# Performance work log

Hardware: AMD Instinct MI355X
Metric: run time of the kernel (lower is better)

## Reference

```python
import jax, jax.numpy as jnp
import numpy as np
import math

B, S, SIG, EMB, LAT, H, L_ENC, L_DEC = 16, 1024, 256, 256, 256, 8, 2, 2
EH, DH = EMB // H, LAT // H
EPS = 1e-10


def _sinusoidal_last_row(d):
    # last row of a standard sinusoidal PE table (position index = max_len-1)
    pos = 5000.0 - 1.0
    i = np.arange(d)
    angles = pos / np.power(10000.0, (2 * (i // 2)) / d)
    pe = np.where(i % 2 == 0, np.sin(angles), np.cos(angles))
    return jnp.asarray(pe, dtype=jnp.float32)


def setup_inputs() -> dict:
    key = jax.random.key(0)
    ks = iter(jax.random.split(key, 64))
    w = lambda *sh: 0.05 * jax.random.normal(next(ks), sh, dtype=jnp.float32)
    z = lambda *sh: jnp.zeros(sh, dtype=jnp.float32)
    d = {
        'inputData': jax.random.normal(next(ks), (B, S, SIG), dtype=jnp.float32),
        'pos_enc': _sinusoidal_last_row(SIG),
        'embW': w(SIG, EMB), 'embb': z(EMB),
        'qW': w(EMB, EMB), 'qb': z(EMB),
        'kW': w(EMB, EMB), 'kb': z(EMB),
        'vW': w(EMB, EMB), 'vb': z(EMB),
        'encBW': w(EH, EH), 'encBb': z(EH),
        'oW': w(EMB, EMB), 'ob': z(EMB),
        'ffe_W1': w(EMB, 2 * EMB), 'ffe_b1': z(2 * EMB),
        'ffe_W2': w(2 * EMB, EMB), 'ffe_b2': z(EMB),
        'lnSA_g': jnp.ones((L_ENC, EMB)), 'lnSA_b': z(L_ENC, EMB),
        'lnFF_g': jnp.ones((L_ENC, EMB)), 'lnFF_b': z(L_ENC, EMB),
        'start': w(1, LAT),
        'decQW': w(LAT, LAT), 'decQb': z(LAT),
        'decKW': w(EMB, EMB), 'decKb': z(EMB),
        'decVW': w(EMB, LAT), 'decVb': z(LAT),
        'decBW': w(EH + DH, DH), 'decBb': z(DH),
        'latW': w(LAT, LAT), 'latb': z(LAT),
        'ffd_W1': w(LAT, LAT // 2), 'ffd_b1': z(LAT // 2),
        'ffd_W2': w(LAT // 2, LAT), 'ffd_b2': z(LAT),
        'lnCA_g': jnp.ones((L_DEC, LAT)), 'lnCA_b': z(L_DEC, LAT),
        'lnLFF_g': jnp.ones((L_DEC, LAT)), 'lnLFF_b': z(L_DEC, LAT),
        'finW': w(LAT, LAT), 'finb': z(LAT),
    }
    return d


def _ln(x, g, b):
    m = x.mean(-1, keepdims=True)
    v = x.var(-1, keepdims=True)
    return (x - m) * jax.lax.rsqrt(v + EPS) * g + b


def _enc_attn(x, qW, qb, kW, kb, vW, vb, bW, bb, oW, ob):
    # x: (B,S,EMB) -> heads (B,H,S,EH)
    sp = lambda t: t.reshape(B, S, H, EH).transpose(0, 2, 1, 3)
    q, k, v = sp(x @ qW + qb), sp(x @ kW + kb), sp(x @ vW + vb)
    bk = k @ bW + bb                                   # bilinear key (B,H,S,EH)
    attn = jax.nn.softmax(jnp.einsum('bhqd,bhkd->bhqk', q, bk) / math.sqrt(EH), axis=-1)
    out = jnp.einsum('bhqk,bhkd->bhqd', attn, v)
    out = out.transpose(0, 2, 1, 3).reshape(B, S, EMB)
    return out @ oW + ob


def _dec_attn(enc, lat, qW, qb, kW, kb, vW, vb, bW, bb, oW, ob):
    # lat: (B,LAT) single query token; enc: (B,S,EMB)
    q = (lat @ qW + qb).reshape(B, 1, H, DH).transpose(0, 2, 1, 3)   # (B,H,1,DH)
    k = (enc @ kW + kb).reshape(B, S, H, EH).transpose(0, 2, 1, 3)   # (B,H,S,EH)
    v = (enc @ vW + vb).reshape(B, S, H, DH).transpose(0, 2, 1, 3)   # (B,H,S,DH)
    qcat = jnp.broadcast_to(q, (B, H, S, DH))
    kcat = jnp.concatenate([k, qcat], axis=-1)                       # (B,H,S,EH+DH)
    bk = kcat @ bW + bb                                              # (B,H,S,DH)
    attn = jax.nn.softmax(jnp.einsum('bhqd,bhkd->bhqk', q, bk) / math.sqrt(EH + DH), axis=-1)
    out = jnp.einsum('bhqk,bhkd->bhqd', attn, v)                     # (B,H,1,DH)
    out = out.transpose(0, 2, 1, 3).reshape(B, LAT)
    return out @ oW + ob


def reference(inputData, pos_enc, embW, embb, qW, qb, kW, kb, vW, vb, encBW, encBb,
              oW, ob, ffe_W1, ffe_b1, ffe_W2, ffe_b2, lnSA_g, lnSA_b, lnFF_g, lnFF_b,
              start, decQW, decQb, decKW, decKb, decVW, decVb, decBW, decBb,
              latW, latb, ffd_W1, ffd_b1, ffd_W2, ffd_b2, lnCA_g, lnCA_b,
              lnLFF_g, lnLFF_b, finW, finb):
    emb = (inputData + pos_enc) @ embW + embb          # (B,S,EMB)
    t = emb
    for l in range(L_ENC):
        n = _ln(t, lnSA_g[l], lnSA_b[l])
        a = _enc_attn(n, qW, qb, kW, kb, vW, vb, encBW, encBb, oW, ob) + n
        t = a + emb
        n2 = _ln(t, lnFF_g[l], lnFF_b[l])
        ff = jax.nn.selu(n2 @ ffe_W1 + ffe_b1) @ ffe_W2 + ffe_b2
        t = ff + n2
    init_lat = jnp.broadcast_to(start, (B, LAT))
    lat = init_lat
    for l in range(L_DEC):
        nl = _ln(init_lat, lnCA_g[l], lnCA_b[l])       # module always feeds initialLatentData
        lat = _dec_attn(t, nl, decQW, decQb, decKW, decKb, decVW, decVb,
                        decBW, decBb, latW, latb)
        nf = _ln(lat, lnLFF_g[l], lnLFF_b[l])
        lat = jax.nn.selu(nf @ ffd_W1 + ffd_b1) @ ffd_W2 + ffd_b2
    return lat @ finW + finb
```

## Files before the change

kernel.cpp:

```cpp
#include <hip/hip_runtime.h>
#include <hip/hip_bf16.h>
#include <math.h>

typedef __hip_bfloat16 bf16;

#define BB 16
#define SS 1024
#define NH 8
#define NR (BB*SS)
#define SZE ((size_t)NR*256)
#define RS 264
#define HS 520
#define KS2 136

typedef __attribute__((ext_vector_type(8))) short short8;
typedef __attribute__((ext_vector_type(4))) float f32x4;
typedef __attribute__((ext_vector_type(8))) unsigned short u16x8;
typedef __attribute__((ext_vector_type(4))) unsigned short u16x4;

__device__ __forceinline__ float bf2f(bf16 x){ return __bfloat162float(x); }
__device__ __forceinline__ bf16  f2bf(float x){ return __float2bfloat16(x); }
__device__ __forceinline__ unsigned short f2bfu(float x){
  bf16 t = __float2bfloat16(x); return *reinterpret_cast<unsigned short*>(&t);
}
__device__ __forceinline__ float bfu2f(unsigned short u){
  return __uint_as_float(((unsigned)u)<<16);
}

__device__ __forceinline__ float ldT(const float* p, size_t i){ return p[i]; }
__device__ __forceinline__ float ldT(const bf16*  p, size_t i){ return bf2f(p[i]); }
__device__ __forceinline__ void  stT(float* p, size_t i, float v){ p[i] = v; }
__device__ __forceinline__ void  stT(bf16*  p, size_t i, float v){ p[i] = f2bf(v); }

__device__ __forceinline__ float selu_f(float x){
  const float a = 1.6732632423543772f, sc = 1.0507009873554805f;
  return sc * (x > 0.f ? x : a * expm1f(x));
}

struct PtrPack { const void* p[43]; };
struct TabPack { int off[43]; int cnt[43]; int total; };
struct TrTab   { int srcOff[12]; int K[12]; int N[12]; int dstOff[12]; int total; };

__global__ __launch_bounds__(256) void k_canon(PtrPack ptrs, TabPack tab,
    float* __restrict__ dst, int* __restrict__ flagw)
{
  unsigned w0 = ((const unsigned*)ptrs.p[18])[0];
  int isbf = (w0 == 0x3F803F80u) ? 1 : 0;
  if (blockIdx.x == 0 && threadIdx.x == 0) *flagw = isbf;
  __shared__ int so[43], sn[43];
  int tid = threadIdx.x;
  if (tid < 43){ so[tid] = tab.off[tid]; sn[tid] = tab.cnt[tid]; }
  __syncthreads();
  int g = blockIdx.x*256 + tid;
  if (g >= tab.total) return;
  int seg = 1;
  while (seg < 42 && g >= so[seg] + sn[seg]) seg++;
  int li = g - so[seg];
  float v = isbf ? bf2f(((const bf16*)ptrs.p[seg])[li])
                 : ((const float*)ptrs.p[seg])[li];
  dst[g] = v;
}

__global__ __launch_bounds__(256) void k_transW(const float* __restrict__ wt,
    TrTab tt, unsigned short* __restrict__ dst)
{
  int g = blockIdx.x*256 + threadIdx.x;
  if (g >= tt.total) return;
  int seg = 0;
  while (seg < 11 && g >= tt.dstOff[seg] + tt.K[seg]*tt.N[seg]) seg++;
  int li = g - tt.dstOff[seg];
  int K = tt.K[seg], N = tt.N[seg];
  int n = li / K, k = li - n*K;
  dst[g] = f2bfu(wt[tt.srcOff[seg] + (size_t)k*N + n]);
}

template<int K, int LDA, int CT>
__device__ __forceinline__ void wave_gemmN(const unsigned short (*As)[LDA],
    const unsigned short* __restrict__ Wt, int n0, f32x4 acc[4][CT], int lane)
{
  int col = lane & 15, quad = lane >> 4;
  #pragma unroll
  for (int k0 = 0; k0 < K; k0 += 32){
    short8 a[4], b[CT];
    #pragma unroll
    for (int rt = 0; rt < 4; rt++)
      a[rt] = *(const short8*)(&As[rt*16 + col][k0 + quad*8]);
    #pragma unroll
    for (int ct = 0; ct < CT; ct++)
      b[ct] = *(const short8*)(&Wt[(size_t)(n0 + ct*16 + col)*K + k0 + quad*8]);
    #pragma unroll
    for (int rt = 0; rt < 4; rt++)
      #pragma unroll
      for (int ct = 0; ct < CT; ct++)
        acc[rt][ct] = __builtin_amdgcn_mfma_f32_16x16x32_bf16(a[rt], b[ct], acc[rt][ct], 0, 0, 0);
  }
}

template<int K, int LDA, int CT>
__device__ __forceinline__ void wave_gemmM32(const unsigned short (*As)[LDA],
    const unsigned short* __restrict__ Wt, int n0, f32x4 acc[2][CT], int lane)
{
  int col = lane & 15, quad = lane >> 4;
  #pragma unroll
  for (int k0 = 0; k0 < K; k0 += 32){
    short8 a[2], b[CT];
    #pragma unroll
    for (int rt = 0; rt < 2; rt++)
      a[rt] = *(const short8*)(&As[rt*16 + col][k0 + quad*8]);
    #pragma unroll
    for (int ct = 0; ct < CT; ct++)
      b[ct] = *(const short8*)(&Wt[(size_t)(n0 + ct*16 + col)*K + k0 + quad*8]);
    #pragma unroll
    for (int rt = 0; rt < 2; rt++)
      #pragma unroll
      for (int ct = 0; ct < CT; ct++)
        acc[rt][ct] = __builtin_amdgcn_mfma_f32_16x16x32_bf16(a[rt], b[ct], acc[rt][ct], 0, 0, 0);
  }
}

#define ZERO_ACC4(acc)  { _Pragma("unroll") for (int rt=0;rt<4;rt++){ _Pragma("unroll") for (int ct=0;ct<4;ct++) acc[rt][ct] = (f32x4){0.f,0.f,0.f,0.f}; } }
#define ZERO_ACC2(acc)  { _Pragma("unroll") for (int rt=0;rt<4;rt++){ _Pragma("unroll") for (int ct=0;ct<2;ct++) acc[rt][ct] = (f32x4){0.f,0.f,0.f,0.f}; } }
#define ZERO_ACC24(acc) { _Pragma("unroll") for (int rt=0;rt<2;rt++){ _Pragma("unroll") for (int ct=0;ct<4;ct++) acc[rt][ct] = (f32x4){0.f,0.f,0.f,0.f}; } }

#define EPI_BEGIN(e) { int rt = (e)>>4, ct = ((e)>>2)&3, r = (e)&3; \
    int lrow = rt*16 + quad*4 + r; int gcol0 = ct*16 + col; \
    float av = acc[rt][ct][r]; (void)lrow; (void)gcol0; (void)av;
#define EPI_END }

#define EPI32_BEGIN(e) { int rt = (e)>>4, ct = ((e)>>2)&3, r = (e)&3; \
    int lrow = rt*16 + quad*4 + r; int gcol0 = ct*16 + col; \
    float av = acc[rt][ct][r]; (void)lrow; (void)gcol0; (void)av;
#define EPI32_END }

template<int PRE, typename OT>
__global__ __launch_bounds__(256) void k_gemm_mfma(const void* __restrict__ A,
    const int* __restrict__ flagp, const float* __restrict__ pe,
    const unsigned short* __restrict__ Wt, const float* __restrict__ bias,
    OT* __restrict__ out)
{
  __shared__ __align__(16) unsigned short As[64][RS];
  int tid = threadIdx.x;
  int m = blockIdx.x & 255, nh = blockIdx.x >> 8;
  int row0 = m*64;
  if (PRE == 0){
    int f = *flagp;
    for (int jj = 0; jj < 64; jj++){
      int idx = tid + jj*256, row = idx>>8, c = idx&255;
      size_t g = (size_t)(row0+row)*256 + c;
      float x = f ? bf2f(((const bf16*)A)[g]) : ((const float*)A)[g];
      As[row][c] = f2bfu(x + pe[c]);
    }
  } else {
    for (int jj = 0; jj < 64; jj++){
      int idx = tid + jj*256, row = idx>>8, c = idx&255;
      As[row][c] = f2bfu(((const float*)A)[(size_t)(row0+row)*256 + c]);
    }
  }
  __syncthreads();
  int w = tid>>6, lane = tid&63, col = lane&15, quad = lane>>4;
  int n0 = nh*128 + w*32;
  f32x4 acc[4][2];
  ZERO_ACC2(acc);
  wave_gemmN<256, RS, 2>(As, Wt, n0, acc, lane);
  #pragma unroll
  for (int rt = 0; rt < 4; rt++){
    #pragma unroll
    for (int ct = 0; ct < 2; ct++){
      #pragma unroll
      for (int r = 0; r < 4; r++){
        int grow = row0 + rt*16 + quad*4 + r;
        int gcol = n0 + ct*16 + col;
        stT(out, (size_t)grow*256 + gcol, acc[rt][ct][r] + bias[gcol]);
      }
    }
  }
}

__global__ __launch_bounds__(256) void k_decKV(const float* __restrict__ A,
    const unsigned short* __restrict__ KWt, const float* __restrict__ kb,
    const unsigned short* __restrict__ VWt, const float* __restrict__ vb,
    bf16* __restrict__ ko, bf16* __restrict__ vo)
{
  __shared__ __align__(16) unsigned short As[64][RS];
  int tid = threadIdx.x;
  int m = blockIdx.x & 255, nh = blockIdx.x >> 8;
  int row0 = m*64;
  for (int jj = 0; jj < 64; jj++){
    int idx = tid + jj*256, row = idx>>8, c = idx&255;
    As[row][c] = f2bfu(A[(size_t)(row0+row)*256 + c]);
  }
  __syncthreads();
  int w = tid>>6, lane = tid&63, col = lane&15, quad = lane>>4;
  int n0 = nh*128 + w*32;
  f32x4 acc[4][2];
  ZERO_ACC2(acc);
  wave_gemmN<256, RS, 2>(As, KWt, n0, acc, lane);
  #pragma unroll
  for (int rt = 0; rt < 4; rt++){
    #pragma unroll
    for (int ct = 0; ct < 2; ct++){
      #pragma unroll
      for (int r = 0; r < 4; r++){
        int grow = row0 + rt*16 + quad*4 + r;
        int gcol = n0 + ct*16 + col;
        ko[(size_t)grow*256 + gcol] = f2bf(acc[rt][ct][r] + kb[gcol]);
      }
    }
  }
  ZERO_ACC2(acc);
  wave_gemmN<256, RS, 2>(As, VWt, n0, acc, lane);
  #pragma unroll
  for (int rt = 0; rt < 4; rt++){
    #pragma unroll
    for (int ct = 0; ct < 2; ct++){
      #pragma unroll
      for (int r = 0; r < 4; r++){
        int grow = row0 + rt*16 + quad*4 + r;
        int gcol = n0 + ct*16 + col;
        vo[(size_t)grow*256 + gcol] = f2bf(acc[rt][ct][r] + vb[gcol]);
      }
    }
  }
}

__global__ __launch_bounds__(256) void k_qkvbk_mfma(const float* __restrict__ tsrc,
    const float* __restrict__ lng, const float* __restrict__ lnb,
    const unsigned short* __restrict__ qWt, const float* __restrict__ qb,
    const unsigned short* __restrict__ kWt, const float* __restrict__ kb,
    const unsigned short* __restrict__ vWt, const float* __restrict__ vb,
    const unsigned short* __restrict__ encBWt, const float* __restrict__ Bb,
    bf16* __restrict__ qo, bf16* __restrict__ vo, bf16* __restrict__ bko)
{
  __shared__ __align__(16) unsigned short Ns[64][RS];
  __shared__ __align__(16) unsigned short Ks[64][KS2];
  __shared__ float mArr[64], rArr[64];
  int tid = threadIdx.x;
  int m = blockIdx.x & 255, nh = blockIdx.x >> 8;
  int row0 = m*64;
  int b = row0 >> 10, s0 = row0 & 1023;
  {
    int row = tid>>2, l4 = tid&3;
    const float* rp = tsrc + (size_t)(row0+row)*256;
    float s = 0.f, s2 = 0.f;
    for (int c = l4; c < 256; c += 4){ float x = rp[c]; s += x; s2 += x*x; }
    s  += __shfl_down(s, 2, 4);  s  += __shfl_down(s, 1, 4);
    s2 += __shfl_down(s2, 2, 4); s2 += __shfl_down(s2, 1, 4);
    if (l4 == 0){
      float mn = s*(1.f/256.f);
      float v = s2*(1.f/256.f) - mn*mn;
      mArr[row] = mn; rArr[row] = rsqrtf(fmaxf(v,0.f) + 1e-10f);
    }
  }
  __syncthreads();
  for (int jj = 0; jj < 64; jj++){
    int idx = tid + jj*256, row = idx>>8, c = idx&255;
    float x = tsrc[(size_t)(row0+row)*256 + c];
    Ns[row][c] = f2bfu((x - mArr[row])*rArr[row]*lng[c] + lnb[c]);
  }
  __syncthreads();
  int w = tid>>6, lane = tid&63, col = lane&15, quad = lane>>4;
  int n0 = nh*128 + w*32;
  f32x4 acc[4][2];
  ZERO_ACC2(acc);
  wave_gemmN<256, RS, 2>(Ns, qWt, n0, acc, lane);
  #pragma unroll
  for (int rt = 0; rt < 4; rt++){
    #pragma unroll
    for (int ct = 0; ct < 2; ct++){
      #pragma unroll
      for (int r = 0; r < 4; r++){
        int grow = row0 + rt*16 + quad*4 + r;
        int gcol = n0 + ct*16 + col;
        qo[(size_t)grow*256 + gcol] = f2bf(acc[rt][ct][r] + qb[gcol]);
      }
    }
  }
  ZERO_ACC2(acc);
  wave_gemmN<256, RS, 2>(Ns, vWt, n0, acc, lane);
  #pragma unroll
  for (int rt = 0; rt < 4; rt++){
    #pragma unroll
    for (int ct = 0; ct < 2; ct++){
      #pragma unroll
      for (int r = 0; r < 4; r++){
        int grow = row0 + rt*16 + quad*4 + r;
        int gcol = n0 + ct*16 + col;
        vo[(size_t)grow*256 + gcol] = f2bf(acc[rt][ct][r] + vb[gcol]);
      }
    }
  }
  ZERO_ACC2(acc);
  wave_gemmN<256, RS, 2>(Ns, kWt, n0, acc, lane);
  #pragma unroll
  for (int rt = 0; rt < 4; rt++){
    #pragma unroll
    for (int ct = 0; ct < 2; ct++){
      #pragma unroll
      for (int r = 0; r < 4; r++){
        int lrow = rt*16 + quad*4 + r;
        int lcol = w*32 + ct*16 + col;
        Ks[lrow][lcol] = f2bfu(acc[rt][ct][r] + kb[nh*128 + lcol]);
      }
    }
  }
  __syncthreads();
  int h = nh*4 + w;
  ZERO_ACC2(acc);
  #pragma unroll
  for (int ct = 0; ct < 2; ct++){
    short8 bfrag = *(const short8*)(&encBWt[(size_t)(ct*16 + col)*32 + quad*8]);
    #pragma unroll
    for (int rt = 0; rt < 4; rt++){
      short8 afrag = *(const short8*)(&Ks[rt*16 + col][w*32 + quad*8]);
      acc[rt][ct] = __builtin_amdgcn_mfma_f32_16x16x32_bf16(afrag, bfrag, acc[rt][ct], 0, 0, 0);
    }
  }
  #pragma unroll
  for (int rt = 0; rt < 4; rt++){
    #pragma unroll
    for (int ct = 0; ct < 2; ct++){
      #pragma unroll
      for (int r = 0; r < 4; r++){
        int srow = s0 + rt*16 + quad*4 + r;
        int d = ct*16 + col;
        bko[(((size_t)(b*NH+h))*SS + srow)*32 + d] = f2bf(acc[rt][ct][r] + Bb[d]);
      }
    }
  }
}

__global__ __launch_bounds__(256) void k_attn_mfma(
    const bf16* __restrict__ q, const bf16* __restrict__ bk,
    const bf16* __restrict__ v, bf16* __restrict__ ao)
{
  int bi = blockIdx.x;
  int qq = bi >> 7, b = (bi >> 3) & 15, h = bi & 7;
  int tid = threadIdx.x;
  int w = tid>>6, lane = tid&63;
  int quad = lane>>4, col = lane&15;
  int q0 = qq*256 + w*64;

  __shared__ __align__(16) unsigned short Ks2b[2][64][32];
  __shared__ __align__(16) unsigned short Vt2b[2][32][72];
  __shared__ __align__(16) unsigned short Ps[4][64][72];

  const float scale2 = 0.17677669529663687f * 1.4426950408889634f;
  short8 aq[4];
  #pragma unroll
  for (int rt = 0; rt < 4; rt++){
    const unsigned short* gq = (const unsigned short*)q
        + ((size_t)(b*SS + q0 + rt*16 + col))*256 + h*32 + quad*8;
    u16x8 qv = *(const u16x8*)gq;
    #pragma unroll
    for (int i=0;i<8;i++) aq[rt][i] = (short)f2bfu(bfu2f(qv[i])*scale2);
  }

  float l_r[4][4];
  f32x4 o0[4], o1[4];
  #pragma unroll
  for (int rt=0;rt<4;rt++){
    o0[rt] = (f32x4){0.f,0.f,0.f,0.f};
    o1[rt] = (f32x4){0.f,0.f,0.f,0.f};
    #pragma unroll
    for (int r=0;r<4;r++) l_r[rt][r] = 0.f;
  }

  u16x8 rK;
  u16x4 rV0, rV1;
  int vk0 = (tid>>3), vdg = (tid&7);
  int vk1 = ((tid+256)>>3), vdg1 = (tid&7);
  {
    const u16x8* srcK = (const u16x8*)((const unsigned short*)bk
        + (((size_t)(b*NH+h))*SS + 0)*32);
    rK = srcK[tid];
    rV0 = *(const u16x4*)((const unsigned short*)v
        + ((size_t)(b*SS + 0 + vk0))*256 + h*32 + vdg*4);
    rV1 = *(const u16x4*)((const unsigned short*)v
        + ((size_t)(b*SS + 0 + vk1))*256 + h*32 + vdg1*4);
  }

  for (int kt = 0; kt < 16; kt++){
    int cb = kt & 1;
    ((u16x8*)&Ks2b[cb][0][0])[tid] = rK;
    #pragma unroll
    for (int i=0;i<4;i++) Vt2b[cb][vdg*4+i][vk0] = rV0[i];
    #pragma unroll
    for (int i=0;i<4;i++) Vt2b[cb][vdg1*4+i][vk1] = rV1[i];
    __syncthreads();
    if (kt < 15){
      int nk = kt + 1;
      const u16x8* srcK = (const u16x8*)((const unsigned short*)bk
          + (((size_t)(b*NH+h))*SS + (size_t)nk*64)*32);
      rK = srcK[tid];
      rV0 = *(const u16x4*)((const unsigned short*)v
          + ((size_t)(b*SS + nk*64 + vk0))*256 + h*32 + vdg*4);
      rV1 = *(const u16x4*)((const unsigned short*)v
          + ((size_t)(b*SS + nk*64 + vk1))*256 + h*32 + vdg1*4);
    }
    short8 bk8[4];
    #pragma unroll
    for (int t4 = 0; t4 < 4; t4++)
      bk8[t4] = *(const short8*)(&Ks2b[cb][t4*16 + col][quad*8]);
    #pragma unroll
    for (int rt = 0; rt < 4; rt++){
      f32x4 s[4];
      #pragma unroll
      for (int t4 = 0; t4 < 4; t4++)
        s[t4] = __builtin_amdgcn_mfma_f32_16x16x32_bf16(aq[rt], bk8[t4],
                  (f32x4){0.f,0.f,0.f,0.f}, 0, 0, 0);
      #pragma unroll
      for (int r=0;r<4;r++){
        #pragma unroll
        for (int t4=0;t4<4;t4++){
          float pv = __builtin_amdgcn_exp2f(s[t4][r]);
          l_r[rt][r] += pv;
          Ps[w][rt*16 + quad*4 + r][t4*16 + col] =
              (unsigned short)(__float_as_uint(pv) >> 16);
        }
      }
    }
    short8 bv00 = *(const short8*)(&Vt2b[cb][col][quad*8]);
    short8 bv10 = *(const short8*)(&Vt2b[cb][col][32 + quad*8]);
    short8 bv01 = *(const short8*)(&Vt2b[cb][16+col][quad*8]);
    short8 bv11 = *(const short8*)(&Vt2b[cb][16+col][32 + quad*8]);
    #pragma unroll
    for (int rt = 0; rt < 4; rt++){
      short8 ap0 = *(const short8*)(&Ps[w][rt*16 + col][quad*8]);
      short8 ap1 = *(const short8*)(&Ps[w][rt*16 + col][32 + quad*8]);
      o0[rt] = __builtin_amdgcn_mfma_f32_16x16x32_bf16(ap0, bv00, o0[rt], 0, 0, 0);
      o0[rt] = __builtin_amdgcn_mfma_f32_16x16x32_bf16(ap1, bv10, o0[rt], 0, 0, 0);
      o1[rt] = __builtin_amdgcn_mfma_f32_16x16x32_bf16(ap0, bv01, o1[rt], 0, 0, 0);
      o1[rt] = __builtin_amdgcn_mfma_f32_16x16x32_bf16(ap1, bv11, o1[rt], 0, 0, 0);
    }
  }
  #pragma unroll
  for (int rt=0;rt<4;rt++){
    #pragma unroll
    for (int r=0;r<4;r++){
      float l = l_r[rt][r];
      #pragma unroll
      for (int msk=1; msk<16; msk<<=1) l += __shfl_xor(l, msk, 64);
      float inv = 1.f / l;
      int qrow = q0 + rt*16 + quad*4 + r;
      size_t o = ((size_t)(b*SS + qrow))*256 + h*32;
      ao[o + col]      = f2bf(o0[rt][r]*inv);
      ao[o + 16 + col] = f2bf(o1[rt][r]*inv);
    }
  }
}

__global__ __launch_bounds__(256) void k_oln_mfma(
    const float* __restrict__ tsrc, const float* __restrict__ emb,
    const bf16* __restrict__ ao,
    const float* __restrict__ lnSAg, const float* __restrict__ lnSAb,
    const unsigned short* __restrict__ oWt, const float* __restrict__ ob,
    const float* __restrict__ lnFFg, const float* __restrict__ lnFFb,
    bf16* __restrict__ n2o)
{
  __shared__ __align__(16) unsigned short Aos[32][RS];
  __shared__ __align__(16) unsigned short Tm[32][RS];
  __shared__ float mArr[32], rArr[32];
  int tid = threadIdx.x, row0 = blockIdx.x*32;
  {
    int row = tid>>3, l8 = tid&7;
    const float* rp = tsrc + (size_t)(row0+row)*256;
    float s = 0.f, s2 = 0.f;
    for (int c = l8; c < 256; c += 8){ float x = rp[c]; s += x; s2 += x*x; }
    s  += __shfl_down(s, 4, 8);  s  += __shfl_down(s, 2, 8);  s  += __shfl_down(s, 1, 8);
    s2 += __shfl_down(s2, 4, 8); s2 += __shfl_down(s2, 2, 8); s2 += __shfl_down(s2, 1, 8);
    if (l8 == 0){
      float m = s*(1.f/256.f);
      float v = s2*(1.f/256.f) - m*m;
      mArr[row] = m; rArr[row] = rsqrtf(fmaxf(v,0.f) + 1e-10f);
    }
  }
  for (int jj = 0; jj < 4; jj++){
    int idx = tid + jj*256;
    int row = idx>>5, c8 = idx&31;
    *(u16x8*)(&Aos[row][c8*8]) =
        *(const u16x8*)((const unsigned short*)ao + (size_t)(row0+row)*256 + c8*8);
  }
  __syncthreads();
  int w = tid>>6, lane = tid&63, col = lane&15, quad = lane>>4;
  f32x4 acc[2][4];
  ZERO_ACC24(acc);
  wave_gemmM32<256, RS, 4>(Aos, oWt, w*64, acc, lane);
  #pragma unroll
  for (int e = 0; e < 32; e++){
    EPI32_BEGIN(e)
    int gcol = w*64 + gcol0;
    size_t g = (size_t)(row0+lrow)*256 + gcol;
    float n1 = (tsrc[g] - mArr[lrow])*rArr[lrow]*lnSAg[gcol] + lnSAb[gcol];
    Tm[lrow][gcol] = f2bfu(av + ob[gcol] + n1 + emb[g]);
    EPI32_END
  }
  __syncthreads();
  {
    int row = tid>>3, l8 = tid&7;
    float s = 0.f, s2 = 0.f;
    for (int c = l8; c < 256; c += 8){ float x = bfu2f(Tm[row][c]); s += x; s2 += x*x; }
    s  += __shfl_down(s, 4, 8);  s  += __shfl_down(s, 2, 8);  s  += __shfl_down(s, 1, 8);
    s2 += __shfl_down(s2, 4, 8); s2 += __shfl_down(s2, 2, 8); s2 += __shfl_down(s2, 1, 8);
    if (l8 == 0){
      float m = s*(1.f/256.f);
      float v = s2*(1.f/256.f) - m*m;
      mArr[row] = m; rArr[row] = rsqrtf(fmaxf(v,0.f) + 1e-10f);
    }
  }
  __syncthreads();
  for (int jj = 0; jj < 32; jj++){
    int idx = tid + jj*256, row = idx>>8, c = idx&255;
    float x = bfu2f(Tm[row][c]);
    n2o[(size_t)(row0+row)*256 + c] =
        f2bf((x - mArr[row])*rArr[row]*lnFFg[c] + lnFFb[c]);
  }
}

__global__ __launch_bounds__(256) void k_ffn_mfma(
    const bf16* __restrict__ n2,
    const unsigned short* __restrict__ W1t, const float* __restrict__ b1,
    const unsigned short* __restrict__ W2t, const float* __restrict__ b2,
    float* __restrict__ tout)
{
  __shared__ __align__(16) unsigned short N2s[32][RS];
  __shared__ __align__(16) unsigned short H1s[32][HS];
  int tid = threadIdx.x, row0 = blockIdx.x*32;
  for (int jj = 0; jj < 4; jj++){
    int idx = tid + jj*256;
    int row = idx>>5, c8 = idx&31;
    *(u16x8*)(&N2s[row][c8*8]) =
        *(const u16x8*)((const unsigned short*)n2 + (size_t)(row0+row)*256 + c8*8);
  }
  __syncthreads();
  int w = tid>>6, lane = tid&63, col = lane&15, quad = lane>>4;
  f32x4 acc[2][4];
  #pragma unroll
  for (int p = 0; p < 2; p++){
    ZERO_ACC24(acc);
    wave_gemmM32<256, RS, 4>(N2s, W1t, p*256 + w*64, acc, lane);
    #pragma unroll
    for (int e = 0; e < 32; e++){
      EPI32_BEGIN(e)
      int gcol = p*256 + w*64 + gcol0;
      H1s[lrow][gcol] = f2bfu(selu_f(av + b1[gcol]));
      EPI32_END
    }
  }
  __syncthreads();
  ZERO_ACC24(acc);
  wave_gemmM32<512, HS, 4>(H1s, W2t, w*64, acc, lane);
  #pragma unroll
  for (int e = 0; e < 32; e++){
    EPI32_BEGIN(e)
    int gcol = w*64 + gcol0;
    tout[(size_t)(row0+lrow)*256 + gcol] = av + b2[gcol] + bfu2f(N2s[lrow][gcol]);
    EPI32_END
  }
}

__global__ __launch_bounds__(256) void k_dec_head(const float* __restrict__ startp,
    const float* __restrict__ lng, const float* __restrict__ lnb,
    const float* __restrict__ decQW, const float* __restrict__ decQb,
    const float* __restrict__ decBW,
    float* __restrict__ s_q, float* __restrict__ s_qc)
{
  __shared__ float s1[256], s2[256], nl[256], qv[256];
  int t = threadIdx.x;
  float v = startp[t];
  s1[t]=v; s2[t]=v*v; __syncthreads();
  for (int s=128;s>0;s>>=1){
    if (t<s){ s1[t]+=s1[t+s]; s2[t]+=s2[t+s]; }
    __syncthreads();
  }
  float m = s1[0]*(1.f/256.f);
  float var = s2[0]*(1.f/256.f) - m*m;
  float r = rsqrtf(fmaxf(var,0.f) + 1e-10f);
  nl[t] = (v-m)*r*lng[t] + lnb[t];
  __syncthreads();
  float acc = decQb[t];
  for (int k=0;k<256;k++) acc += nl[k]*decQW[k*256+t];
  qv[t] = acc; s_q[t] = acc;
  __syncthreads();
  int h = t>>5, d = t&31;
  float a = 0.f;
  #pragma unroll 8
  for (int e=0;e<32;e++) a += qv[h*32+e]*decBW[(32+e)*32 + d];
  s_qc[t] = a;
}

__global__ __launch_bounds__(256) void k_bkdec_mfma(const bf16* __restrict__ kk,
    const float* __restrict__ qc, const unsigned short* __restrict__ decBWt,
    const float* __restrict__ Bb, bf16* __restrict__ bko)
{
  __shared__ __align__(16) unsigned short Ks[64][RS];
  int tid = threadIdx.x, row0 = blockIdx.x*64;
  int b = row0 >> 10, s0 = row0 & 1023;
  for (int jj = 0; jj < 8; jj++){
    int idx = tid + jj*256;
    int row = idx>>5, c8 = idx&31;
    *(u16x8*)(&Ks[row][c8*8]) =
        *(const u16x8*)((const unsigned short*)kk + (size_t)(row0+row)*256 + c8*8);
  }
  __syncthreads();
  int w = tid>>6, lane = tid&63, col = lane&15, quad = lane>>4;
  f32x4 acc[4][4];
  ZERO_ACC4(acc);
  #pragma unroll
  for (int ct = 0; ct < 4; ct++){
    int base = w*64 + ct*16;
    int h = base >> 5, d0 = base & 31;
    short8 bfrag = *(const short8*)(&decBWt[(size_t)(d0 + col)*32 + quad*8]);
    #pragma unroll
    for (int rt = 0; rt < 4; rt++){
      short8 afrag = *(const short8*)(&Ks[rt*16 + col][h*32 + quad*8]);
      acc[rt][ct] = __builtin_amdgcn_mfma_f32_16x16x32_bf16(afrag, bfrag, acc[rt][ct], 0, 0, 0);
    }
  }
  #pragma unroll
  for (int e = 0; e < 64; e++){
    EPI_BEGIN(e)
    int srow = s0 + lrow;
    int gcol = w*64 + gcol0;
    int h = gcol >> 5, d = gcol & 31;
    bko[(((size_t)(b*NH+h))*SS + srow)*32 + d] = f2bf(av + qc[gcol] + Bb[d]);
    EPI_END
  }
}

__global__ __launch_bounds__(256) void k_attn_dec(const float* __restrict__ q,
    const bf16* __restrict__ bk, const bf16* __restrict__ v,
    float* __restrict__ out)
{
  int h = blockIdx.x & 7, b = blockIdx.x >> 3;
  int tid = threadIdx.x;
  __shared__ float qs[32];
  __shared__ float sc[SS];
  __shared__ float red[256];
  if (tid < 32) qs[tid] = q[h*32 + tid] * (0.125f * 1.4426950408889634f);
  __syncthreads();
  float lsum = 0.f;
  for (int jj=0;jj<4;jj++){
    int j = tid*4 + jj;
    size_t base = (((size_t)(b*NH+h))*SS + j)*32;
    float s = 0.f;
    #pragma unroll
    for (int d=0;d<32;d++) s += qs[d]*bf2f(bk[base + d]);
    float e = __builtin_amdgcn_exp2f(s);
    sc[j] = e; lsum += e;
  }
  red[tid] = lsum; __syncthreads();
  for (int s=128;s>0;s>>=1){ if (tid<s) red[tid]+=red[tid+s]; __syncthreads(); }
  float gs = red[0];
  __syncthreads();
  int d = tid & 31, c = tid >> 5;
  float acc = 0.f;
  for (int j=c*128; j<c*128+128; j++)
    acc += sc[j]*bf2f(v[((size_t)(b*SS + j))*256 + h*32 + d]);
  red[c*32+d] = acc;
  __syncthreads();
  if (tid < 32){
    float s = 0.f;
    #pragma unroll
    for (int cc=0;cc<8;cc++) s += red[cc*32+tid];
    out[b*256 + h*32 + tid] = s / gs;
  }
}

__global__ __launch_bounds__(256) void k_dec_tail(const float* __restrict__ s_ao,
    const float* __restrict__ latW, const float* __restrict__ latb,
    const float* __restrict__ lng, const float* __restrict__ lnb,
    const float* __restrict__ W1, const float* __restrict__ b1,
    const float* __restrict__ W2, const float* __restrict__ b2,
    const float* __restrict__ finW, const float* __restrict__ finb,
    const int* __restrict__ flagp, void* __restrict__ outv)
{
  __shared__ float x[256], y[256], s1[256], s2[256];
  int t = threadIdx.x, b = blockIdx.x;
  x[t] = s_ao[b*256 + t];
  __syncthreads();
  float lat = latb[t];
  for (int k=0;k<256;k++) lat += x[k]*latW[k*256+t];
  s1[t]=lat; s2[t]=lat*lat; __syncthreads();
  for (int s=128;s>0;s>>=1){
    if (t<s){ s1[t]+=s1[t+s]; s2[t]+=s2[t+s]; }
    __syncthreads();
  }
  float m = s1[0]*(1.f/256.f);
  float var = s2[0]*(1.f/256.f) - m*m;
  float r = rsqrtf(fmaxf(var,0.f) + 1e-10f);
  y[t] = (lat-m)*r*lng[t] + lnb[t];
  __syncthreads();
  if (t < 128){
    float a2 = b1[t];
    for (int k=0;k<256;k++) a2 += y[k]*W1[k*128+t];
    x[t] = selu_f(a2);
  }
  __syncthreads();
  float a3 = b2[t];
  for (int k=0;k<128;k++) a3 += x[k]*W2[k*256+t];
  s1[t] = a3;
  __syncthreads();
  float o = finb[t];
  for (int k=0;k<256;k++) o += s1[k]*finW[k*256+t];
  size_t oi = (size_t)b*256 + t;
  if (*flagp) ((bf16*)outv)[oi] = f2bf(o);
  else        ((float*)outv)[oi] = o;
}

extern "C" void kernel_launch(void* const* d_in, const int* in_sizes, int n_in,
                              void* d_out, int out_size, void* d_ws, size_t ws_size,
                              hipStream_t stream)
{
  static const int cnts[43] = {
    0,256,65536,256,65536,256,65536,256,65536,256,1024,32,65536,256,
    131072,512,131072,256,512,512,512,512,256,65536,256,65536,256,65536,256,
    2048,32,65536,256,32768,128,32768,256,512,512,512,512,65536,256 };
  TabPack tab; int acc0 = 0;
  for (int i = 0; i < 43; i++){ tab.off[i] = acc0; tab.cnt[i] = cnts[i]; acc0 += cnts[i]; }
  tab.total = acc0;
  PtrPack ptrs;
  for (int i = 0; i < 43; i++) ptrs.p[i] = d_in[i];

  char* p = (char*)d_ws;
  float* wt   = (float*)p;
  int*  flagp = (int*)(p + (4u<<20));
  char* bigc  = p + (4u<<20) + 256;
  float* g_emb = (float*)bigc;
  float* g_t   = (float*)(bigc + SZE*4);
  bf16*  g_q   = (bf16*)(bigc + 2*SZE*4);
  bf16*  g_v   = (bf16*)(bigc + 2*SZE*4 + SZE*2);
  bf16*  g_ao  = (bf16*)(bigc + 2*SZE*4 + 2*SZE*2);
  bf16*  g_bk  = (bf16*)(bigc + 2*SZE*4 + 3*SZE*2);
  float* fsm   = (float*)(bigc + 2*SZE*4 + 4*SZE*2);
  unsigned short* wtr = (unsigned short*)(bigc + 2*SZE*4 + 4*SZE*2 + 131072*4);
  float* s_q  = fsm;
  float* s_qc = fsm + 256;
  float* s_ao = fsm + 512;

  static const int trIdx[10] = {2,4,6,8,12,14,16,25,27,10};
  static const int trK[10]   = {256,256,256,256,256,256,512,256,256,32};
  static const int trN[10]   = {256,256,256,256,256,512,256,256,256,32};
  TrTab tr; int tacc = 0;
  for (int i = 0; i < 10; i++){
    tr.srcOff[i] = tab.off[trIdx[i]];
    tr.K[i] = trK[i]; tr.N[i] = trN[i];
    tr.dstOff[i] = tacc; tacc += trK[i]*trN[i];
  }
  tr.srcOff[10] = tab.off[29];        tr.K[10]=32; tr.N[10]=32; tr.dstOff[10]=tacc; tacc+=1024;
  tr.srcOff[11] = tab.off[29] + 1024; tr.K[11]=32; tr.N[11]=32; tr.dstOff[11]=tacc; tacc+=1024;
  tr.total = tacc;
  const unsigned short *embWt = wtr + tr.dstOff[0], *qWt = wtr + tr.dstOff[1],
    *kWt = wtr + tr.dstOff[2], *vWt = wtr + tr.dstOff[3], *oWt = wtr + tr.dstOff[4],
    *ffeW1t = wtr + tr.dstOff[5], *ffeW2t = wtr + tr.dstOff[6],
    *decKWt = wtr + tr.dstOff[7], *decVWt = wtr + tr.dstOff[8],
    *encBWt = wtr + tr.dstOff[9], *decBWtk = wtr + tr.dstOff[10];

  #define WP(i) (wt + tab.off[i])
  const float *pe=WP(1), *embb=WP(3), *qb=WP(5), *kb=WP(7), *vb=WP(9),
    *encBb=WP(11), *ob=WP(13), *ffeb1=WP(15), *ffeb2=WP(17),
    *lnSAg=WP(18), *lnSAb=WP(19), *lnFFg=WP(20), *lnFFb=WP(21),
    *startp=WP(22), *decQW=WP(23), *decQb=WP(24), *decKb=WP(26),
    *decVb=WP(28), *decBW=WP(29), *decBb=WP(30), *latW=WP(31),
    *latb=WP(32), *ffdW1=WP(33), *ffdb1=WP(34), *ffdW2=WP(35), *ffdb2=WP(36),
    *lnCAg=WP(37), *lnCAb=WP(38), *lnLFFg=WP(39), *lnLFFb=WP(40),
    *finW=WP(41), *finb=WP(42);

  dim3 blk(256);
  const int G64  = NR/64;
  const int G32  = NR/32;
  const int GSP  = 512;
  const int GA2  = 512;
  const int LD   = 1;

  k_canon<<<(tab.total+255)/256, blk, 0, stream>>>(ptrs, tab, wt, flagp);
  k_transW<<<(tr.total+255)/256, blk, 0, stream>>>(wt, tr, wtr);

  k_gemm_mfma<0,float><<<GSP, blk, 0, stream>>>(d_in[0], flagp, pe, embWt, embb, g_emb);

  const float* tcur = g_emb;
  for (int l = 0; l < 2; l++){
    k_qkvbk_mfma<<<GSP, blk, 0, stream>>>(tcur, lnSAg+l*256, lnSAb+l*256,
        qWt, qb, kWt, kb, vWt, vb, encBWt, encBb, g_q, g_v, g_bk);
    k_attn_mfma<<<GA2, blk, 0, stream>>>(g_q, g_bk, g_v, g_ao);
    k_oln_mfma<<<G32, blk, 0, stream>>>(tcur, g_emb, g_ao,
        lnSAg+l*256, lnSAb+l*256, oWt, ob, lnFFg+l*256, lnFFb+l*256, g_q);
    k_ffn_mfma<<<G32, blk, 0, stream>>>(g_q, ffeW1t, ffeb1, ffeW2t, ffeb2, g_t);
    tcur = g_t;
  }

  k_dec_head<<<1, blk, 0, stream>>>(startp, lnCAg+LD*256, lnCAb+LD*256,
      decQW, decQb, decBW, s_q, s_qc);
  k_decKV<<<GSP, blk, 0, stream>>>(g_t, decKWt, decKb, decVWt, decVb, g_q, g_v);
  k_bkdec_mfma<<<G64, blk, 0, stream>>>(g_q, s_qc, decBWtk, decBb, g_bk);
  k_attn_dec<<<BB*NH, blk, 0, stream>>>(s_q, g_bk, g_v, s_ao);
  k_dec_tail<<<BB, blk, 0, stream>>>(s_ao, latW, latb, lnLFFg+LD*256, lnLFFb+LD*256,
      ffdW1, ffdb1, ffdW2, ffdb2, finW, finb, flagp, d_out);
  #undef WP
}
```

Measured before the change: 549.6 us.

## Split encoder FFN into two double-buffered LDS-DMA tiled GEMM kernels

Replaces the fused per-32-row FFN kernel with two separate tiled GEMM launches (128x64 tiles) that write the hidden activation to global memory in between. Each launch double-buffers K tiles in LDS using global_load_lds with an XOR swizzle, and blocks are remapped so that neighbouring blocks share weight tiles. The goal is better MFMA utilisation and overlap of loads with compute than the fused kernel, which restreamed the full weights for every 32 rows. The cost is an extra round trip of the 16K x 512 bf16 intermediate through HBM and one more kernel launch.

Result: faster. 514.0 us (-6.5%).

```diff
diff --git a/kernel.cpp b/kernel.cpp
--- a/kernel.cpp
+++ b/kernel.cpp
@@ -35,6 +35,12 @@
 __device__ __forceinline__ float selu_f(float x){
   const float a = 1.6732632423543772f, sc = 1.0507009873554805f;
   return sc * (x > 0.f ? x : a * expm1f(x));
+}
+
+__device__ __forceinline__ void gload16(const void* g, void* l){
+  __builtin_amdgcn_global_load_lds(
+      (const __attribute__((address_space(1))) unsigned int*)g,
+      (__attribute__((address_space(3))) unsigned int*)l, 16, 0, 0);
 }
 
 struct PtrPack { const void* p[43]; };
@@ -516,45 +522,95 @@
   }
 }
 
-__global__ __launch_bounds__(256) void k_ffn_mfma(
-    const bf16* __restrict__ n2,
-    const unsigned short* __restrict__ W1t, const float* __restrict__ b1,
-    const unsigned short* __restrict__ W2t, const float* __restrict__ b2,
-    float* __restrict__ tout)
-{
-  __shared__ __align__(16) unsigned short N2s[32][RS];
-  __shared__ __align__(16) unsigned short H1s[32][HS];
-  int tid = threadIdx.x, row0 = blockIdx.x*32;
-  for (int jj = 0; jj < 4; jj++){
-    int idx = tid + jj*256;
-    int row = idx>>5, c8 = idx&31;
-    *(u16x8*)(&N2s[row][c8*8]) =
-        *(const u16x8*)((const unsigned short*)n2 + (size_t)(row0+row)*256 + c8*8);
-  }
-  __syncthreads();
-  int w = tid>>6, lane = tid&63, col = lane&15, quad = lane>>4;
-  f32x4 acc[2][4];
-  #pragma unroll
-  for (int p = 0; p < 2; p++){
-    ZERO_ACC24(acc);
-    wave_gemmM32<256, RS, 4>(N2s, W1t, p*256 + w*64, acc, lane);
-    #pragma unroll
-    for (int e = 0; e < 32; e++){
-      EPI32_BEGIN(e)
-      int gcol = p*256 + w*64 + gcol0;
-      H1s[lrow][gcol] = f2bfu(selu_f(av + b1[gcol]));
-      EPI32_END
-    }
-  }
-  __syncthreads();
-  ZERO_ACC24(acc);
-  wave_gemmM32<512, HS, 4>(H1s, W2t, w*64, acc, lane);
-  #pragma unroll
-  for (int e = 0; e < 32; e++){
-    EPI32_BEGIN(e)
-    int gcol = w*64 + gcol0;
-    tout[(size_t)(row0+lrow)*256 + gcol] = av + b2[gcol] + bfu2f(N2s[lrow][gcol]);
-    EPI32_END
+#define FF_STAGE(B, KT) { \
+  int k0 = (KT)*64; \
+  _Pragma("unroll") \
+  for (int i = 0; i < 4; i++){ int c = w*4 + i; \
+    gload16(A  + (size_t)(row0 + c*8 + rsub)*KFULL + k0 + sgo, &As[B][c*512]); } \
+  _Pragma("unroll") \
+  for (int i = 0; i < 2; i++){ int c = w*2 + i; \
+    gload16(Wb + (size_t)(n0   + c*8 + rsub)*KFULL + k0 + sgo, &Bs[B][c*512]); } }
+
+#define FF_COMPUTE(B) { \
+  _Pragma("unroll") \
+  for (int kk = 0; kk < 2; kk++){ \
+    short8 a[4], b2r[2]; \
+    _Pragma("unroll") \
+    for (int rt = 0; rt < 4; rt++) \
+      a[rt] = *(const short8*)(&As[B][((wr*64 + rt*16 + col)<<6) + ((((kk<<2)|quad) ^ (col&7))<<3)]); \
+    _Pragma("unroll") \
+    for (int ct = 0; ct < 2; ct++) \
+      b2r[ct] = *(const short8*)(&Bs[B][((wc*32 + ct*16 + col)<<6) + ((((kk<<2)|quad) ^ (col&7))<<3)]); \
+    _Pragma("unroll") \
+    for (int rt = 0; rt < 4; rt++) \
+      _Pragma("unroll") \
+      for (int ct = 0; ct < 2; ct++) \
+        acc[rt][ct] = __builtin_amdgcn_mfma_f32_16x16x32_bf16(a[rt], b2r[ct], acc[rt][ct], 0, 0, 0); } }
+
+template<int KFULL, int NFULL, int EPI>
+__global__ __launch_bounds__(256) void k_ff_gemm(const bf16* __restrict__ A,
+    const unsigned short* __restrict__ Wt, const float* __restrict__ bias,
+    const bf16* __restrict__ res, void* __restrict__ outv)
+{
+  __shared__ __align__(16) unsigned short As[2][128*64];
+  __shared__ __align__(16) unsigned short Bs[2][64*64];
+  constexpr int NWG = 128 * (NFULL/64);
+  constexpr int NKT = KFULL/64;
+  int tid = threadIdx.x;
+  int w = tid>>6, lane = tid&63;
+  int col = lane&15, quad = lane>>4;
+  int wr = w>>1, wc = w&1;
+  int rsub = lane>>3;
+  int sgo = (((lane&7) ^ rsub)<<3);
+  int bid = blockIdx.x;
+  int swz = (bid & 7)*(NWG>>3) + (bid >> 3);
+  int mb = swz & 127, nb = swz >> 7;
+  int row0 = mb*128, n0 = nb*64;
+  const bf16* Wb = (const bf16*)Wt;
+
+  f32x4 acc[4][2];
+  ZERO_ACC2(acc);
+
+  FF_STAGE(0, 0);
+  __syncthreads();
+  #pragma unroll
+  for (int kt = 0; kt < NKT-1; kt++){
+    int cb = kt & 1;
+    FF_STAGE(cb^1, kt+1);
+    FF_COMPUTE(cb);
+    __syncthreads();
+  }
+  FF_COMPUTE((NKT-1)&1);
+
+  if (EPI == 0){
+    bf16* o = (bf16*)outv;
+    #pragma unroll
+    for (int rt = 0; rt < 4; rt++){
+      #pragma unroll
+      for (int ct = 0; ct < 2; ct++){
+        #pragma unroll
+        for (int r = 0; r < 4; r++){
+          int grow = row0 + wr*64 + rt*16 + quad*4 + r;
+          int gcol = n0 + wc*32 + ct*16 + col;
+          o[(size_t)grow*NFULL + gcol] = f2bf(selu_f(acc[rt][ct][r] + bias[gcol]));
+        }
+      }
+    }
+  } else {
+    float* o = (float*)outv;
+    #pragma unroll
+    for (int rt = 0; rt < 4; rt++){
+      #pragma unroll
+      for (int ct = 0; ct < 2; ct++){
+        #pragma unroll
+        for (int r = 0; r < 4; r++){
+          int grow = row0 + wr*64 + rt*16 + quad*4 + r;
+          int gcol = n0 + wc*32 + ct*16 + col;
+          size_t g = (size_t)grow*NFULL + gcol;
+          o[g] = acc[rt][ct][r] + bias[gcol] + bf2f(res[g]);
+        }
+      }
+    }
   }
 }
 
@@ -736,6 +792,7 @@
   float* s_q  = fsm;
   float* s_qc = fsm + 256;
   float* s_ao = fsm + 512;
+  bf16*  g_h1 = g_v;
 
   static const int trIdx[10] = {2,4,6,8,12,14,16,25,27,10};
   static const int trK[10]   = {256,256,256,256,256,256,512,256,256,32};
@@ -784,7 +841,8 @@
     k_attn_mfma<<<GA2, blk, 0, stream>>>(g_q, g_bk, g_v, g_ao);
     k_oln_mfma<<<G32, blk, 0, stream>>>(tcur, g_emb, g_ao,
         lnSAg+l*256, lnSAb+l*256, oWt, ob, lnFFg+l*256, lnFFb+l*256, g_q);
-    k_ffn_mfma<<<G32, blk, 0, stream>>>(g_q, ffeW1t, ffeb1, ffeW2t, ffeb2, g_t);
+    k_ff_gemm<256,512,0><<<1024, blk, 0, stream>>>(g_q, ffeW1t, ffeb1, (const bf16*)nullptr, g_h1);
+    k_ff_gemm<512,256,1><<<512, blk, 0, stream>>>(g_h1, ffeW2t, ffeb2, g_q, g_t);
     tcur = g_t;
   }
 
```
